# Optimization experiments

Hardware: AMD Instinct MI355X
Metric: run time of the kernel (lower is better)

The kernel has to match this reference:

```python
import jax, jax.numpy as jnp
import numpy as np


def setup_inputs() -> dict:
    key = jax.random.key(0)
    ks = jax.random.split(key, 10)
    B, L, H, T = 512, 30, 1024, 30
    k = 1.0 / np.sqrt(H).astype(np.float32)
    input_hidden = jax.random.normal(ks[0], (B, L, H), jnp.float32)
    tgt = jax.random.normal(ks[1], (B, T, H), jnp.float32)
    # all entries valid (no -1 padding): guarantees every row always has an
    # unmasked slot so softmax never sees an all -inf row (the torch code NaNs there)
    pos_label = jax.random.randint(ks[2], (B, L), 0, L)
    S = jax.random.uniform(ks[3], (H,), jnp.float32)            # torch.rand init
    W_ih = jax.random.uniform(ks[4], (3 * H, H), jnp.float32, -k, k)
    W_hh = jax.random.uniform(ks[5], (3 * H, H), jnp.float32, -k, k)
    b_ih = jax.random.uniform(ks[6], (3 * H,), jnp.float32, -k, k)
    b_hh = jax.random.uniform(ks[7], (3 * H,), jnp.float32, -k, k)
    Wl_w = jax.random.uniform(ks[8], (H, H), jnp.float32, -k, k)
    Wl_b = jax.random.uniform(ks[9], (H,), jnp.float32, -k, k)
    return dict(input_hidden=input_hidden, tgt=tgt, pos_label=pos_label,
                max_length=30, S=S, W_ih=W_ih, W_hh=W_hh, b_ih=b_ih, b_hh=b_hh,
                Wl_w=Wl_w, Wl_b=Wl_b)


def reference(input_hidden, tgt, pos_label, max_length, S, W_ih, W_hh, b_ih, b_hh, Wl_w, Wl_b):
    # teacher_forcing_ratio = 1.0, generate = False (training path of Plan_GRU)
    B, L, H = input_hidden.shape
    T = max_length
    ss = (pos_label != -1).sum(axis=1)                     # [B] valid prefix length
    valid = jnp.arange(L)[None, :] < ss[:, None]           # [B, L]

    def gru_cell(x, h):
        gi = x @ W_ih.T + b_ih                             # [B, 3H]
        gh = h @ W_hh.T + b_hh
        ir, iz, inn = jnp.split(gi, 3, axis=-1)
        hr, hz, hn = jnp.split(gh, 3, axis=-1)
        r = jax.nn.sigmoid(ir + hr)
        z = jax.nn.sigmoid(iz + hz)
        n = jnp.tanh(inn + r * hn)
        return (1.0 - z) * n + z * h

    h0 = input_hidden.mean(axis=1)                         # [B, H]
    x0 = jnp.broadcast_to(S, (B, H))
    # input at step 0 is S; at step i>0 it is tgt[:, i-1] (teacher forcing)
    xs = jnp.concatenate([x0[:, None, :], tgt[:, :T - 1]], axis=1).transpose(1, 0, 2)  # [T,B,H]
    flag0 = jnp.zeros((B, L), jnp.bool_)

    def step(carry, x):
        h, flag = carry
        h = gru_cell(x, h)                                 # [B, H]
        pre = jnp.einsum('bh,blh->bl', h @ Wl_w.T + Wl_b, input_hidden)  # [B, L]
        masked = jnp.where(flag | ~valid, -jnp.inf, jax.lax.stop_gradient(pre))
        top = jax.nn.softmax(masked, axis=1)
        am = jnp.argmax(top, axis=1)                       # [B]
        flag = flag | (jnp.arange(L)[None, :] == am[:, None])
        return (h, flag), (pre, top)

    (_, _), (preds, infer) = jax.lax.scan(step, (h0, flag0), xs)
    outputs = preds.transpose(1, 0, 2)                     # [B, T, L]
    pre_inf = jax.lax.stop_gradient(infer.transpose(1, 0, 2))
    return outputs, pre_inf
```

## Files before the change

### kernel.cpp

```cpp
#include <hip/hip_runtime.h>

#define Bsz 512
#define Lsz 30
#define Hsz 1024
#define Tsz 30

typedef _Float16 f16;
typedef f16 f16x8 __attribute__((ext_vector_type(8)));
typedef unsigned short u16x8 __attribute__((ext_vector_type(8)));
typedef float  f32x4  __attribute__((ext_vector_type(4)));
typedef unsigned int u32;
typedef unsigned short u16;

#define WSCALE 32.0f
#define INVWS  0.03125f
#define INV2   0.0009765625f

__device__ __forceinline__ u16 h2u(f16 h) {
  union { f16 h; u16 u; } v; v.h = h; return v.u;
}
__device__ __forceinline__ f16x8 ld8h(const u16* p) {
  return *reinterpret_cast<const f16x8*>(p);
}
__device__ __forceinline__ void stage16(const u16* g, u16* l) {
  __builtin_amdgcn_global_load_lds(
      (const __attribute__((address_space(1))) u32*)g,
      (__attribute__((address_space(3))) u32*)l, 16, 0, 0);
}

__global__ __launch_bounds__(256) void k_split(
    const float* __restrict__ src, u16* __restrict__ hi,
    u16* __restrict__ lo, int n4)
{
  const int i = blockIdx.x * 256 + threadIdx.x;
  if (i >= n4) return;
  const float4 v = ((const float4*)src)[i];
  const float f[4] = { v.x * WSCALE, v.y * WSCALE, v.z * WSCALE, v.w * WSCALE };
  u16 h[4], l[4];
  #pragma unroll
  for (int j = 0; j < 4; ++j) {
    const f16 hb = (f16)f[j];
    const f16 lb = (f16)(f[j] - (float)hb);
    h[j] = h2u(hb); l[j] = h2u(lb);
  }
  ((ushort4*)hi)[i] = make_ushort4(h[0], h[1], h[2], h[3]);
  ((ushort4*)lo)[i] = make_ushort4(l[0], l[1], l[2], l[3]);
}

__global__ __launch_bounds__(256) void k_splitT2(
    const float* __restrict__ src, u16* __restrict__ t0, u16* __restrict__ t1)
{
  __shared__ float t[32][33];
  const int tid = threadIdx.x;
  const int bi = blockIdx.x * 32, bj = blockIdx.y * 32;
  const int r = tid >> 3, c4 = (tid & 7) * 4;
  const float4 v = *(const float4*)(src + (size_t)(bi + r) * Hsz + bj + c4);
  t[r][c4] = v.x; t[r][c4 + 1] = v.y; t[r][c4 + 2] = v.z; t[r][c4 + 3] = v.w;
  __syncthreads();
  u16 h[4], l[4];
  #pragma unroll
  for (int i = 0; i < 4; ++i) {
    const float f = t[c4 + i][r] * WSCALE;
    const f16 hb = (f16)f;
    const f16 lb = (f16)(f - (float)hb);
    h[i] = h2u(hb); l[i] = h2u(lb);
  }
  const size_t o = (size_t)(bj + r) * Hsz + bi + c4;
  *(ushort4*)(t0 + o) = make_ushort4(h[0], h[1], h[2], h[3]);
  *(ushort4*)(t1 + o) = make_ushort4(l[0], l[1], l[2], l[3]);
}

__global__ __launch_bounds__(256) void k_init(
    const float* __restrict__ ih, const int* __restrict__ pos,
    const float* __restrict__ wlb,
    float* __restrict__ hf, u16* __restrict__ hh,
    u16* __restrict__ hl, float* __restrict__ c0,
    u32* __restrict__ valid)
{
  __shared__ float red[4];
  const int b = blockIdx.x, tid = threadIdx.x;
  const int lane = tid & 63, wid = tid >> 6;
  const float4 wb = ((const float4*)wlb)[tid];
  float s0 = 0.f, s1 = 0.f, s2 = 0.f, s3 = 0.f;
  for (int l = 0; l < Lsz; ++l) {
    const float4 v = ((const float4*)(ih + ((size_t)b * Lsz + l) * Hsz))[tid];
    s0 += v.x; s1 += v.y; s2 += v.z; s3 += v.w;
    float part = v.x * wb.x + v.y * wb.y + v.z * wb.z + v.w * wb.w;
    #pragma unroll
    for (int off = 32; off >= 1; off >>= 1) part += __shfl_xor(part, off, 64);
    if (lane == 0) red[wid] = part;
    __syncthreads();
    if (tid == 0) c0[b * Lsz + l] = red[0] + red[1] + red[2] + red[3];
    __syncthreads();
  }
  const size_t o = (size_t)b * Hsz + tid * 4;
  const float m[4] = { s0 / 30.f, s1 / 30.f, s2 / 30.f, s3 / 30.f };
  *(float4*)(hf + o) = make_float4(m[0], m[1], m[2], m[3]);
  u16 h4[4], l4[4];
  #pragma unroll
  for (int j = 0; j < 4; ++j) {
    const float hs = m[j] * WSCALE;
    const f16 hb = (f16)hs;
    const f16 lb = (f16)(hs - (float)hb);
    h4[j] = h2u(hb); l4[j] = h2u(lb);
  }
  *(ushort4*)(hh + o) = make_ushort4(h4[0], h4[1], h4[2], h4[3]);
  *(ushort4*)(hl + o) = make_ushort4(l4[0], l4[1], l4[2], l4[3]);
  if (tid == 0) {
    int ss = 0;
    for (int l = 0; l < Lsz; ++l) ss += (pos[b * Lsz + l] != -1) ? 1 : 0;
    valid[b] = (ss >= 32) ? 0xFFFFFFFFu : ((1u << ss) - 1u);
  }
}

__global__ __launch_bounds__(256) void k_gemv0(
    const float* __restrict__ S, const float* __restrict__ wih,
    float* __restrict__ gi0)
{
  const int n = blockIdx.x * 64 + (threadIdx.x >> 2);
  const int part = threadIdx.x & 3;
  const float4* s4 = (const float4*)S + part * 64;
  const float4* w4 = (const float4*)(wih + (size_t)n * Hsz) + part * 64;
  float s = 0.f;
  #pragma unroll 8
  for (int i = 0; i < 64; ++i) {
    const float4 a = s4[i], b = w4[i];
    s = fmaf(a.x, b.x, s); s = fmaf(a.y, b.y, s);
    s = fmaf(a.z, b.z, s); s = fmaf(a.w, b.w, s);
  }
  s += __shfl_xor(s, 1, 64);
  s += __shfl_xor(s, 2, 64);
  if (part == 0) gi0[n] = s;
}

template<int MODE>
__global__ __launch_bounds__(256) void k_tgemm(
    const float* __restrict__ Afp,
    const u16* __restrict__ Bh, const u16* __restrict__ Bl,
    float* __restrict__ C, u16* __restrict__ Ch, u16* __restrict__ Cl,
    int ldc, int t0)
{
  constexpr int oAh = 0, oAl = 4096, oBh = 8192, oBl = 12288;
  __shared__ u16 lds[2][16384];

  const int tid = threadIdx.x;
  const int w = tid >> 6, lane = tid & 63;
  const int wm = w >> 1, wn = w & 1;
  const int lr = lane & 15, lg = lane >> 4;

  const int nwg = gridDim.x * gridDim.y;
  int lin = blockIdx.y * gridDim.x + blockIdx.x;
  lin = (lin & 7) * (nwg >> 3) + (lin >> 3);
  const int bm = (lin / gridDim.x) * 128, bn = (lin % gridDim.x) * 128;

  const int ar = tid & 127, kh = tid >> 7;
  long arow;
  if (MODE == 1) arow = (long)((bm + ar) & 511) * Tsz + (t0 - 1) + ((bm + ar) >> 9);
  else           arow = bm + ar;
  const float* aptr = Afp + arow * Hsz + kh * 16;
  const int awo0 = (ar >> 4) * 512 + ((ar & 15) + 32 * kh) * 8;

  const u16* gpB[4]; int bwo[4];
  #pragma unroll
  for (int i = 0; i < 4; ++i) {
    const int cid = (w << 2) | i;
    const u16* base; int g, off;
    if (cid < 8) { base = Bh; g = cid;     off = oBh + g * 512; }
    else         { base = Bl; g = cid - 8; off = oBl + g * 512; }
    gpB[i] = base + (size_t)(bn + g * 16 + lr) * Hsz + lg * 8;
    bwo[i] = off;
  }

  float4 areg[4];
  #define LOAD_A() { _Pragma("unroll") for (int i = 0; i < 4; ++i) areg[i] = ((const float4*)aptr)[i]; aptr += 32; }
  #define STAGE_B(buf) { _Pragma("unroll") for (int i = 0; i < 4; ++i) { stage16(gpB[i], &lds[buf][bwo[i]]); gpB[i] += 32; } }
  #define WRITE_A(buf) { \
    u16x8 h0v, h1v, l0v, l1v; \
    _Pragma("unroll") for (int i = 0; i < 4; ++i) { \
      const float f[4] = { areg[i].x, areg[i].y, areg[i].z, areg[i].w }; \
      _Pragma("unroll") for (int c = 0; c < 4; ++c) { \
        const int j = 4 * i + c; \
        const f16 hb = (f16)f[c]; \
        const f16 lb = (f16)(f[c] - (float)hb); \
        if (j < 8) { h0v[j] = h2u(hb); l0v[j] = h2u(lb); } \
        else       { h1v[j - 8] = h2u(hb); l1v[j - 8] = h2u(lb); } \
      } \
    } \
    *(u16x8*)&lds[buf][oAh + awo0]       = h0v; \
    *(u16x8*)&lds[buf][oAh + awo0 + 128] = h1v; \
    *(u16x8*)&lds[buf][oAl + awo0]       = l0v; \
    *(u16x8*)&lds[buf][oAl + awo0 + 128] = l1v; }

  f32x4 acc[4][4] = {};

  LOAD_A();
  STAGE_B(0);
  WRITE_A(0);
  __syncthreads();

  for (int ks = 0; ks < 32; ++ks) {
    const int cur = ks & 1;
    if (ks < 31) { STAGE_B(cur ^ 1); LOAD_A(); }
    {
      const u16* L = &lds[cur][0];
      f16x8 a_h[4], a_l[4], b_h[4], b_l[4];
      #pragma unroll
      for (int m = 0; m < 4; ++m) {
        const int g = wm * 4 + m;
        a_h[m] = ld8h(L + oAh + g * 512 + lane * 8);
        a_l[m] = ld8h(L + oAl + g * 512 + lane * 8);
      }
      #pragma unroll
      for (int n = 0; n < 4; ++n) {
        const int g = wn * 4 + n;
        b_h[n] = ld8h(L + oBh + g * 512 + lane * 8);
        b_l[n] = ld8h(L + oBl + g * 512 + lane * 8);
      }
      #pragma unroll
      for (int m = 0; m < 4; ++m)
        #pragma unroll
        for (int n = 0; n < 4; ++n) {
          acc[m][n] = __builtin_amdgcn_mfma_f32_16x16x32_f16(a_h[m], b_h[n], acc[m][n], 0, 0, 0);
          acc[m][n] = __builtin_amdgcn_mfma_f32_16x16x32_f16(a_h[m], b_l[n], acc[m][n], 0, 0, 0);
          acc[m][n] = __builtin_amdgcn_mfma_f32_16x16x32_f16(a_l[m], b_h[n], acc[m][n], 0, 0, 0);
        }
    }
    __syncthreads();
    if (ks < 31) { WRITE_A(cur ^ 1); __syncthreads(); }
  }

  #pragma unroll
  for (int n = 0; n < 4; ++n) {
    const int col = bn + wn * 64 + n * 16 + lr;
    #pragma unroll
    for (int m = 0; m < 4; ++m) {
      #pragma unroll
      for (int rr = 0; rr < 4; ++rr) {
        const int row = bm + wm * 64 + m * 16 + lg * 4 + rr;
        if (MODE == 1) {
          const int slot = (t0 + (row >> 9)) & 7;
          C[((size_t)slot * Bsz + (row & 511)) * 3072 + col] = acc[m][n][rr] * INVWS;
        } else {
          const float v = acc[m][n][rr];
          const f16 hb = (f16)v;
          const f16 lb = (f16)(v - (float)hb);
          Ch[(size_t)row * ldc + col] = h2u(hb);
          Cl[(size_t)row * ldc + col] = h2u(lb);
        }
      }
    }
  }
  #undef LOAD_A
  #undef STAGE_B
  #undef WRITE_A
}

__global__ __launch_bounds__(512) void k_ghc(
    const u16* __restrict__ Hh, const u16* __restrict__ Hl,
    const u16* __restrict__ Wh, const u16* __restrict__ Wl,
    const float* __restrict__ gi, int gi_rs,
    const float* __restrict__ bih, const float* __restrict__ bhh,
    const float* __restrict__ hf_in, float* __restrict__ hf_out,
    u16* __restrict__ hho, u16* __restrict__ hlo,
    u16* __restrict__ Hph, u16* __restrict__ Hpl, int tstep)
{
  constexpr int oAh = 0, oAl = 2048, oBh = 4096, oBl = 7168;
  __shared__ u16 lds[2][10240];

  const int bn = (blockIdx.x & 31) * 32, bm = (blockIdx.x >> 5) * 64;
  const int tid = threadIdx.x;
  const int w = tid >> 6, lane = tid & 63;
  const int wm = w >> 1, wn = w & 1;
  const int lr = lane & 15, lg = lane >> 4;

  const u16* gp[3]; int ldso[3];
  const int nch = (w < 4) ? 3 : 2;
  #pragma unroll
  for (int i = 0; i < 3; ++i) {
    const int cid = w + 8 * i;
    if (cid >= 20) break;
    const u16* base; long row; int off;
    if (cid < 4)       { const int g = cid;      row = bm + g * 16 + lr;                         base = Hh; off = oAh + g * 512; }
    else if (cid < 8)  { const int g = cid - 4;  row = bm + g * 16 + lr;                         base = Hl; off = oAl + g * 512; }
    else if (cid < 14) { const int g = cid - 8;  row = (g >> 1) * 1024 + bn + (g & 1) * 16 + lr; base = Wh; off = oBh + g * 512; }
    else               { const int g = cid - 14; row = (g >> 1) * 1024 + bn + (g & 1) * 16 + lr; base = Wl; off = oBl + g * 512; }
    gp[i] = base + row * Hsz + lg * 8;
    ldso[i] = off;
  }

  f32x4 acc[3] = {};

  for (int i = 0; i < nch; ++i) { stage16(gp[i], &lds[0][ldso[i]]); gp[i] += 32; }
  __syncthreads();

  for (int ks = 0; ks < 32; ++ks) {
    const int cur = ks & 1;
    if (ks < 31) {
      for (int i = 0; i < nch; ++i) { stage16(gp[i], &lds[cur ^ 1][ldso[i]]); gp[i] += 32; }
    }
    const u16* L = &lds[cur][0];
    const f16x8 ah = ld8h(L + oAh + wm * 512 + lane * 8);
    const f16x8 al = ld8h(L + oAl + wm * 512 + lane * 8);
    #pragma unroll
    for (int gt = 0; gt < 3; ++gt) {
      const int g = gt * 2 + wn;
      const f16x8 bh = ld8h(L + oBh + g * 512 + lane * 8);
      const f16x8 bl = ld8h(L + oBl + g * 512 + lane * 8);
      acc[gt] = __builtin_amdgcn_mfma_f32_16x16x32_f16(ah, bh, acc[gt], 0, 0, 0);
      acc[gt] = __builtin_amdgcn_mfma_f32_16x16x32_f16(ah, bl, acc[gt], 0, 0, 0);
      acc[gt] = __builtin_amdgcn_mfma_f32_16x16x32_f16(al, bh, acc[gt], 0, 0, 0);
    }
    __syncthreads();
  }

  const int c = bn + wn * 16 + lr;
  const float b_ir = bih[c], b_iz = bih[1024 + c], b_in = bih[2048 + c];
  const float b_hr = bhh[c], b_hz = bhh[1024 + c], b_hn = bhh[2048 + c];
  #pragma unroll
  for (int rr = 0; rr < 4; ++rr) {
    const int row = bm + wm * 16 + lg * 4 + rr;
    const size_t gr = (size_t)row * gi_rs;
    const float pr = gi[gr + c]        + b_ir + acc[0][rr] * INV2 + b_hr;
    const float pz = gi[gr + 1024 + c] + b_iz + acc[1][rr] * INV2 + b_hz;
    const float r = 1.f / (1.f + expf(-pr));
    const float z = 1.f / (1.f + expf(-pz));
    const float n = tanhf(gi[gr + 2048 + c] + b_in + r * (acc[2][rr] * INV2 + b_hn));
    const size_t o = (size_t)row * Hsz + c;
    const float h = (1.f - z) * n + z * hf_in[o];
    hf_out[o] = h;
    const float hs = h * WSCALE;
    const f16 hb = (f16)hs;
    const f16 lb = (f16)(hs - (float)hb);
    hho[o] = h2u(hb);
    hlo[o] = h2u(lb);
    const size_t o2 = ((size_t)row * Tsz + tstep) * Hsz + c;
    Hph[o2] = h2u(hb);
    Hpl[o2] = h2u(lb);
  }
}

__global__ __launch_bounds__(256) void k_pre(
    const u16* __restrict__ Hph, const u16* __restrict__ Hpl,
    const u16* __restrict__ Gh, const u16* __restrict__ Gl,
    float* __restrict__ P)
{
  const int b = blockIdx.x;
  const int w = threadIdx.x >> 6, lane = threadIdx.x & 63;
  const int wm = w >> 1, wn = w & 1;
  const int lr = lane & 15, lg = lane >> 4;

  const int t_ = wm * 16 + lr;
  const int l_ = wn * 16 + lr;
  const size_t abase = ((size_t)b * Tsz + t_) * Hsz + lg * 8;
  const size_t bbase = ((size_t)b * Tsz + l_) * Hsz + lg * 8;

  f32x4 acc = {};
  for (int k0 = 0; k0 < Hsz; k0 += 32) {
    const f16x8 ah = ld8h(Hph + abase + k0);
    const f16x8 al = ld8h(Hpl + abase + k0);
    const f16x8 bh = ld8h(Gh + bbase + k0);
    const f16x8 bl = ld8h(Gl + bbase + k0);
    acc = __builtin_amdgcn_mfma_f32_16x16x32_f16(ah, bh, acc, 0, 0, 0);
    acc = __builtin_amdgcn_mfma_f32_16x16x32_f16(ah, bl, acc, 0, 0, 0);
    acc = __builtin_amdgcn_mfma_f32_16x16x32_f16(al, bh, acc, 0, 0, 0);
  }

  #pragma unroll
  for (int rr = 0; rr < 4; ++rr) {
    const int tr = wm * 16 + lg * 4 + rr;
    P[(size_t)b * 1024 + tr * 32 + wn * 16 + lr] = acc[rr] * INV2;
  }
}

__global__ __launch_bounds__(64) void k_sm(
    const float* __restrict__ P, const float* __restrict__ c0,
    const u32* __restrict__ valid, float* __restrict__ out)
{
  const int b = blockIdx.x;
  const int l = threadIdx.x;
  const bool act = (l < Lsz);
  const float c0l = act ? c0[b * Lsz + l] : 0.f;
  const u32 vmask = valid[b];
  u32 fl = 0;

  for (int t = 0; t < Tsz; ++t) {
    const float pre = act ? (P[(size_t)b * 1024 + t * 32 + l] + c0l) : 0.f;
    if (act) out[(size_t)b * (Tsz * Lsz) + t * Lsz + l] = pre;
    const u32 ex = fl | ~vmask;
    const bool ok = act && !((ex >> l) & 1u);
    const float v = ok ? pre : -3.4e38f;
    float best = v;
    #pragma unroll
    for (int off = 32; off >= 1; off >>= 1) best = fmaxf(best, __shfl_xor(best, off, 64));
    const unsigned long long msk = __ballot(v == best);
    const int am = __ffsll((long long)msk) - 1;
    const float e = ok ? expf(pre - best) : 0.f;
    float sum = e;
    #pragma unroll
    for (int off = 32; off >= 1; off >>= 1) sum += __shfl_xor(sum, off, 64);
    if (act)
      out[(size_t)Bsz * Tsz * Lsz + (size_t)b * (Tsz * Lsz) + t * Lsz + l] = e / sum;
    fl |= (1u << am);
  }
}

extern "C" void kernel_launch(void* const* d_in, const int* in_sizes, int n_in,
                              void* d_out, int out_size, void* d_ws, size_t ws_size,
                              hipStream_t stream) {
  const float* ih  = (const float*)d_in[0];
  const float* tg  = (const float*)d_in[1];
  const int*   pos = (const int*)d_in[2];
  const float* S   = (const float*)d_in[4];
  const float* wih = (const float*)d_in[5];
  const float* whh = (const float*)d_in[6];
  const float* bih = (const float*)d_in[7];
  const float* bhh = (const float*)d_in[8];
  const float* wlw = (const float*)d_in[9];
  const float* wlb = (const float*)d_in[10];
  float* out = (float*)d_out;

  const size_t NW3 = (size_t)3 * Hsz * Hsz;
  const size_t NW1 = (size_t)Hsz * Hsz;
  const size_t NH  = (size_t)Bsz * Hsz;
  const size_t NPL = ((size_t)Bsz * Tsz + 2) * Hsz;

  char* p = (char*)d_ws;
  u16* wihh = (u16*)p; p += NW3 * 2;
  u16* wihl = (u16*)p; p += NW3 * 2;
  u16* whhh = (u16*)p; p += NW3 * 2;
  u16* whhl = (u16*)p; p += NW3 * 2;
  u16* wlt0 = (u16*)p; p += NW1 * 2;
  u16* wlt1 = (u16*)p; p += NW1 * 2;
  float* ring = (float*)p; p += (size_t)8 * Bsz * 3072 * 4;
  u16* Gh  = (u16*)p; p += NPL * 2;
  u16* Gl  = (u16*)p; p += NPL * 2;
  u16* Hph = (u16*)p; p += NPL * 2;
  u16* Hpl = (u16*)p; p += NPL * 2;
  float* P   = (float*)p; p += (size_t)Bsz * 1024 * 4;
  float* c0  = (float*)p; p += (size_t)Bsz * Lsz * 4;
  float* gi0 = (float*)p; p += 3072 * 4;
  float* hfb[2]; u16* hhb[2]; u16* hlb[2];
  hfb[0] = (float*)p; p += NH * 4;
  hfb[1] = (float*)p; p += NH * 4;
  hhb[0] = (u16*)p; p += NH * 2;
  hlb[0] = (u16*)p; p += NH * 2;
  hhb[1] = (u16*)p; p += NH * 2;
  hlb[1] = (u16*)p; p += NH * 2;
  u32* valid = (u32*)p; p += Bsz * 4;

  k_split<<<(int)(NW3 / 4 + 255) / 256, 256, 0, stream>>>(wih, wihh, wihl, (int)(NW3 / 4));
  k_split<<<(int)(NW3 / 4 + 255) / 256, 256, 0, stream>>>(whh, whhh, whhl, (int)(NW3 / 4));
  k_splitT2<<<dim3(32, 32), 256, 0, stream>>>(wlw, wlt0, wlt1);
  k_init<<<Bsz, 256, 0, stream>>>(ih, pos, wlb, hfb[0], hhb[0], hlb[0], c0, valid);
  k_gemv0<<<48, 256, 0, stream>>>(S, wih, gi0);
  k_tgemm<0><<<dim3(8, 120), 256, 0, stream>>>(ih, wlt0, wlt1, nullptr, Gh, Gl, Hsz, 0);

  k_ghc<<<256, 512, 0, stream>>>(hhb[0], hlb[0], whhh, whhl, gi0, 0, bih, bhh,
                                 hfb[0], hfb[1], hhb[1], hlb[1], Hph, Hpl, 0);

  for (int t = 1; t < Tsz; ++t) {
    if (t == 1 || t == 9 || t == 17 || t == 25) {
      const int ns = (t == 25) ? 5 : 8;
      k_tgemm<1><<<dim3(24, ns * 4), 256, 0, stream>>>(tg, wihh, wihl, ring,
                                                       nullptr, nullptr, 3072, t);
    }
    const int ci = t & 1, ni = (t + 1) & 1;
    k_ghc<<<256, 512, 0, stream>>>(hhb[ci], hlb[ci], whhh, whhl,
                                   ring + (size_t)(t & 7) * Bsz * 3072, 3072,
                                   bih, bhh, hfb[ci], hfb[ni], hhb[ni], hlb[ni],
                                   Hph, Hpl, t);
  }

  k_pre<<<Bsz, 256, 0, stream>>>(Hph, Hpl, Gh, Gl, P);
  k_sm<<<Bsz, 64, 0, stream>>>(P, c0, valid, out);
}
```

Before: 1.701 ms.

## Fuse next-step input-gate GEMM into the recurrent GRU step kernel

Replaces the batched per-8-step input-projection GEMM launches with a combined step kernel. Blocks 0-255 run the recurrent hidden GEMM and GRU update for step t, and 96 extra blocks compute the input gates for step t+1 into the ring buffer. The aim is to fill idle CUs during the latency-bound recurrent step and remove separate large GEMM launches. In exchange the LDS allocation grows to the larger 16384-element buffer for all blocks, which may reduce occupancy of the recurrent blocks.

```diff
diff --git a/kernel.cpp b/kernel.cpp
--- a/kernel.cpp
+++ b/kernel.cpp
@@ -133,12 +133,10 @@
   if (part == 0) gi0[n] = s;
 }
 
-template<int MODE>
-__global__ __launch_bounds__(256) void k_tgemm(
+__global__ __launch_bounds__(256) void k_gemmG(
     const float* __restrict__ Afp,
     const u16* __restrict__ Bh, const u16* __restrict__ Bl,
-    float* __restrict__ C, u16* __restrict__ Ch, u16* __restrict__ Cl,
-    int ldc, int t0)
+    u16* __restrict__ Ch, u16* __restrict__ Cl)
 {
   constexpr int oAh = 0, oAl = 4096, oBh = 8192, oBl = 12288;
   __shared__ u16 lds[2][16384];
@@ -154,10 +152,7 @@
   const int bm = (lin / gridDim.x) * 128, bn = (lin % gridDim.x) * 128;
 
   const int ar = tid & 127, kh = tid >> 7;
-  long arow;
-  if (MODE == 1) arow = (long)((bm + ar) & 511) * Tsz + (t0 - 1) + ((bm + ar) >> 9);
-  else           arow = bm + ar;
-  const float* aptr = Afp + arow * Hsz + kh * 16;
+  const float* aptr = Afp + (size_t)(bm + ar) * Hsz + kh * 16;
   const int awo0 = (ar >> 4) * 512 + ((ar & 15) + 32 * kh) * 8;
 
   const u16* gpB[4]; int bwo[4];
@@ -237,16 +232,11 @@
       #pragma unroll
       for (int rr = 0; rr < 4; ++rr) {
         const int row = bm + wm * 64 + m * 16 + lg * 4 + rr;
-        if (MODE == 1) {
-          const int slot = (t0 + (row >> 9)) & 7;
-          C[((size_t)slot * Bsz + (row & 511)) * 3072 + col] = acc[m][n][rr] * INVWS;
-        } else {
-          const float v = acc[m][n][rr];
-          const f16 hb = (f16)v;
-          const f16 lb = (f16)(v - (float)hb);
-          Ch[(size_t)row * ldc + col] = h2u(hb);
-          Cl[(size_t)row * ldc + col] = h2u(lb);
-        }
+        const float v = acc[m][n][rr];
+        const f16 hb = (f16)v;
+        const f16 lb = (f16)(v - (float)hb);
+        Ch[(size_t)row * Hsz + col] = h2u(hb);
+        Cl[(size_t)row * Hsz + col] = h2u(lb);
       }
     }
   }
@@ -255,7 +245,8 @@
   #undef WRITE_A
 }
 
-__global__ __launch_bounds__(512) void k_ghc(
+__device__ __forceinline__ void ghc_body(
+    u16 (*lds)[16384],
     const u16* __restrict__ Hh, const u16* __restrict__ Hl,
     const u16* __restrict__ Wh, const u16* __restrict__ Wl,
     const float* __restrict__ gi, int gi_rs,
@@ -265,8 +256,6 @@
     u16* __restrict__ Hph, u16* __restrict__ Hpl, int tstep)
 {
   constexpr int oAh = 0, oAl = 2048, oBh = 4096, oBl = 7168;
-  __shared__ u16 lds[2][10240];
-
   const int bn = (blockIdx.x & 31) * 32, bm = (blockIdx.x >> 5) * 64;
   const int tid = threadIdx.x;
   const int w = tid >> 6, lane = tid & 63;
@@ -336,6 +325,120 @@
     const size_t o2 = ((size_t)row * Tsz + tstep) * Hsz + c;
     Hph[o2] = h2u(hb);
     Hpl[o2] = h2u(lb);
+  }
+}
+
+__device__ __forceinline__ void gi_body(
+    u16 (*lds)[16384],
+    const float* __restrict__ tg,
+    const u16* __restrict__ Bh, const u16* __restrict__ Bl,
+    float* __restrict__ ring, int ts, int gb)
+{
+  constexpr int oAh = 0, oAl = 4096, oBh = 8192, oBl = 12288;
+  const int tid = threadIdx.x;
+  const int w = tid >> 6, lane = tid & 63;
+  const int wm = w & 1, wn = w >> 1;
+  const int lr = lane & 15, lg = lane >> 4;
+  const int bm = (gb / 24) * 128, bn = (gb % 24) * 128;
+
+  const int ar = tid & 127, kh = tid >> 7;
+  const float* aptr = tg + ((size_t)(bm + ar) * Tsz + (ts - 1)) * Hsz + kh * 8;
+  const int awo = (ar >> 4) * 512 + ((ar & 15) + 16 * kh) * 8;
+
+  const u16* gpB[2]; int bwo[2];
+  #pragma unroll
+  for (int i = 0; i < 2; ++i) {
+    const int cid = w * 2 + i;
+    const u16* base; int g, off;
+    if (cid < 8) { base = Bh; g = cid;     off = oBh + g * 512; }
+    else         { base = Bl; g = cid - 8; off = oBl + g * 512; }
+    gpB[i] = base + (size_t)(bn + g * 16 + lr) * Hsz + lg * 8;
+    bwo[i] = off;
+  }
+
+  float4 a0, a1;
+  #define GI_LOAD_A() { a0 = ((const float4*)aptr)[0]; a1 = ((const float4*)aptr)[1]; aptr += 32; }
+  #define GI_STAGE_B(buf) { _Pragma("unroll") for (int i = 0; i < 2; ++i) { stage16(gpB[i], &lds[buf][bwo[i]]); gpB[i] += 32; } }
+  #define GI_WRITE_A(buf) { \
+    u16x8 hv, lv; \
+    const float f[8] = { a0.x, a0.y, a0.z, a0.w, a1.x, a1.y, a1.z, a1.w }; \
+    _Pragma("unroll") for (int j = 0; j < 8; ++j) { \
+      const f16 hb = (f16)f[j]; \
+      const f16 lb = (f16)(f[j] - (float)hb); \
+      hv[j] = h2u(hb); lv[j] = h2u(lb); \
+    } \
+    *(u16x8*)&lds[buf][oAh + awo] = hv; \
+    *(u16x8*)&lds[buf][oAl + awo] = lv; }
+
+  f32x4 acc[4][2] = {};
+
+  GI_LOAD_A();
+  GI_STAGE_B(0);
+  GI_WRITE_A(0);
+  __syncthreads();
+
+  for (int ks = 0; ks < 32; ++ks) {
+    const int cur = ks & 1;
+    if (ks < 31) { GI_STAGE_B(cur ^ 1); GI_LOAD_A(); }
+    {
+      const u16* L = &lds[cur][0];
+      f16x8 a_h[4], a_l[4], b_h[2], b_l[2];
+      #pragma unroll
+      for (int m = 0; m < 4; ++m) {
+        const int g = wm * 4 + m;
+        a_h[m] = ld8h(L + oAh + g * 512 + lane * 8);
+        a_l[m] = ld8h(L + oAl + g * 512 + lane * 8);
+      }
+      #pragma unroll
+      for (int n = 0; n < 2; ++n) {
+        const int g = wn * 2 + n;
+        b_h[n] = ld8h(L + oBh + g * 512 + lane * 8);
+        b_l[n] = ld8h(L + oBl + g * 512 + lane * 8);
+      }
+      #pragma unroll
+      for (int m = 0; m < 4; ++m)
+        #pragma unroll
+        for (int n = 0; n < 2; ++n) {
+          acc[m][n] = __builtin_amdgcn_mfma_f32_16x16x32_f16(a_h[m], b_h[n], acc[m][n], 0, 0, 0);
+          acc[m][n] = __builtin_amdgcn_mfma_f32_16x16x32_f16(a_h[m], b_l[n], acc[m][n], 0, 0, 0);
+          acc[m][n] = __builtin_amdgcn_mfma_f32_16x16x32_f16(a_l[m], b_h[n], acc[m][n], 0, 0, 0);
+        }
+    }
+    __syncthreads();
+    if (ks < 31) { GI_WRITE_A(cur ^ 1); __syncthreads(); }
+  }
+
+  const int slot = ts & 7;
+  #pragma unroll
+  for (int n = 0; n < 2; ++n) {
+    const int col = bn + wn * 32 + n * 16 + lr;
+    #pragma unroll
+    for (int m = 0; m < 4; ++m) {
+      #pragma unroll
+      for (int rr = 0; rr < 4; ++rr) {
+        const int row = bm + wm * 64 + m * 16 + lg * 4 + rr;
+        ring[((size_t)slot * Bsz + row) * 3072 + col] = acc[m][n][rr] * INVWS;
+      }
+    }
+  }
+  #undef GI_LOAD_A
+  #undef GI_STAGE_B
+  #undef GI_WRITE_A
+}
+
+__global__ __launch_bounds__(512) void k_step(
+    const u16* hh_t, const u16* hl_t, const u16* Wh, const u16* Wl,
+    const float* gi, int gi_rs, const float* bih, const float* bhh,
+    const float* hf_in, float* hf_out, u16* hh_n, u16* hl_n,
+    u16* Hph, u16* Hpl,
+    const float* tg, const u16* Wih_h, const u16* Wih_l, float* ring, int t)
+{
+  __shared__ u16 lds[2][16384];
+  if (blockIdx.x < 256) {
+    ghc_body(lds, hh_t, hl_t, Wh, Wl, gi, gi_rs, bih, bhh,
+             hf_in, hf_out, hh_n, hl_n, Hph, Hpl, t);
+  } else if (t + 1 < Tsz) {
+    gi_body(lds, tg, Wih_h, Wih_l, ring, t + 1, blockIdx.x - 256);
   }
 }
 
@@ -453,22 +556,16 @@
   k_splitT2<<<dim3(32, 32), 256, 0, stream>>>(wlw, wlt0, wlt1);
   k_init<<<Bsz, 256, 0, stream>>>(ih, pos, wlb, hfb[0], hhb[0], hlb[0], c0, valid);
   k_gemv0<<<48, 256, 0, stream>>>(S, wih, gi0);
-  k_tgemm<0><<<dim3(8, 120), 256, 0, stream>>>(ih, wlt0, wlt1, nullptr, Gh, Gl, Hsz, 0);
-
-  k_ghc<<<256, 512, 0, stream>>>(hhb[0], hlb[0], whhh, whhl, gi0, 0, bih, bhh,
-                                 hfb[0], hfb[1], hhb[1], hlb[1], Hph, Hpl, 0);
-
-  for (int t = 1; t < Tsz; ++t) {
-    if (t == 1 || t == 9 || t == 17 || t == 25) {
-      const int ns = (t == 25) ? 5 : 8;
-      k_tgemm<1><<<dim3(24, ns * 4), 256, 0, stream>>>(tg, wihh, wihl, ring,
-                                                       nullptr, nullptr, 3072, t);
-    }
+  k_gemmG<<<dim3(8, 120), 256, 0, stream>>>(ih, wlt0, wlt1, Gh, Gl);
+
+  for (int t = 0; t < Tsz; ++t) {
     const int ci = t & 1, ni = (t + 1) & 1;
-    k_ghc<<<256, 512, 0, stream>>>(hhb[ci], hlb[ci], whhh, whhl,
-                                   ring + (size_t)(t & 7) * Bsz * 3072, 3072,
-                                   bih, bhh, hfb[ci], hfb[ni], hhb[ni], hlb[ni],
-                                   Hph, Hpl, t);
+    const float* gip = (t == 0) ? gi0 : (ring + (size_t)(t & 7) * Bsz * 3072);
+    k_step<<<352, 512, 0, stream>>>(hhb[ci], hlb[ci], whhh, whhl,
+                                    gip, (t == 0) ? 0 : 3072, bih, bhh,
+                                    hfb[ci], hfb[ni], hhb[ni], hlb[ni],
+                                    Hph, Hpl,
+                                    tg, wihh, wihl, ring, t);
   }
 
   k_pre<<<Bsz, 256, 0, stream>>>(Hph, Hpl, Gh, Gl, P);
```

Measured after the change: 2.109 ms. 24.0% more time.

## Fuse input-gate GEMM into per-step GRU kernel and drop precomputed ring buffer

Applied to the files above, without the earlier changes.

Removes the batched input-projection GEMM (k_tgemm MODE 1) that wrote fp32 gate inputs into a ring buffer, and the step-0 GEMV. Each per-step GRU kernel now computes both x@W_ih and h@W_hh with split-fp16 MFMAs. A-operands are loaded straight from global memory into registers with prefetch, and only weights are staged in LDS. The tgt tensor is pre-split into fp16 hi/lo once, and S is broadcast into a hi/lo buffer. This removes ring-buffer traffic and extra launches, but doubles the MFMA work and the weight streaming inside the serial recurrent loop.

```diff
diff --git a/kernel.cpp b/kernel.cpp
--- a/kernel.cpp
+++ b/kernel.cpp
@@ -68,6 +68,24 @@
   const size_t o = (size_t)(bj + r) * Hsz + bi + c4;
   *(ushort4*)(t0 + o) = make_ushort4(h[0], h[1], h[2], h[3]);
   *(ushort4*)(t1 + o) = make_ushort4(l[0], l[1], l[2], l[3]);
+}
+
+__global__ __launch_bounds__(256) void k_x0(
+    const float* __restrict__ S, u16* __restrict__ xh, u16* __restrict__ xl)
+{
+  const int b = blockIdx.x, tid = threadIdx.x;
+  const float4 v = ((const float4*)S)[tid];
+  const float f[4] = { v.x * WSCALE, v.y * WSCALE, v.z * WSCALE, v.w * WSCALE };
+  u16 h[4], l[4];
+  #pragma unroll
+  for (int j = 0; j < 4; ++j) {
+    const f16 hb = (f16)f[j];
+    const f16 lb = (f16)(f[j] - (float)hb);
+    h[j] = h2u(hb); l[j] = h2u(lb);
+  }
+  const size_t o = (size_t)b * Hsz + tid * 4;
+  *(ushort4*)(xh + o) = make_ushort4(h[0], h[1], h[2], h[3]);
+  *(ushort4*)(xl + o) = make_ushort4(l[0], l[1], l[2], l[3]);
 }
 
 __global__ __launch_bounds__(256) void k_init(
@@ -113,32 +131,10 @@
   }
 }
 
-__global__ __launch_bounds__(256) void k_gemv0(
-    const float* __restrict__ S, const float* __restrict__ wih,
-    float* __restrict__ gi0)
-{
-  const int n = blockIdx.x * 64 + (threadIdx.x >> 2);
-  const int part = threadIdx.x & 3;
-  const float4* s4 = (const float4*)S + part * 64;
-  const float4* w4 = (const float4*)(wih + (size_t)n * Hsz) + part * 64;
-  float s = 0.f;
-  #pragma unroll 8
-  for (int i = 0; i < 64; ++i) {
-    const float4 a = s4[i], b = w4[i];
-    s = fmaf(a.x, b.x, s); s = fmaf(a.y, b.y, s);
-    s = fmaf(a.z, b.z, s); s = fmaf(a.w, b.w, s);
-  }
-  s += __shfl_xor(s, 1, 64);
-  s += __shfl_xor(s, 2, 64);
-  if (part == 0) gi0[n] = s;
-}
-
-template<int MODE>
-__global__ __launch_bounds__(256) void k_tgemm(
+__global__ __launch_bounds__(256) void k_gemmG(
     const float* __restrict__ Afp,
     const u16* __restrict__ Bh, const u16* __restrict__ Bl,
-    float* __restrict__ C, u16* __restrict__ Ch, u16* __restrict__ Cl,
-    int ldc, int t0)
+    u16* __restrict__ Ch, u16* __restrict__ Cl)
 {
   constexpr int oAh = 0, oAl = 4096, oBh = 8192, oBl = 12288;
   __shared__ u16 lds[2][16384];
@@ -154,10 +150,7 @@
   const int bm = (lin / gridDim.x) * 128, bn = (lin % gridDim.x) * 128;
 
   const int ar = tid & 127, kh = tid >> 7;
-  long arow;
-  if (MODE == 1) arow = (long)((bm + ar) & 511) * Tsz + (t0 - 1) + ((bm + ar) >> 9);
-  else           arow = bm + ar;
-  const float* aptr = Afp + arow * Hsz + kh * 16;
+  const float* aptr = Afp + (size_t)(bm + ar) * Hsz + kh * 16;
   const int awo0 = (ar >> 4) * 512 + ((ar & 15) + 32 * kh) * 8;
 
   const u16* gpB[4]; int bwo[4];
@@ -237,16 +230,11 @@
       #pragma unroll
       for (int rr = 0; rr < 4; ++rr) {
         const int row = bm + wm * 64 + m * 16 + lg * 4 + rr;
-        if (MODE == 1) {
-          const int slot = (t0 + (row >> 9)) & 7;
-          C[((size_t)slot * Bsz + (row & 511)) * 3072 + col] = acc[m][n][rr] * INVWS;
-        } else {
-          const float v = acc[m][n][rr];
-          const f16 hb = (f16)v;
-          const f16 lb = (f16)(v - (float)hb);
-          Ch[(size_t)row * ldc + col] = h2u(hb);
-          Cl[(size_t)row * ldc + col] = h2u(lb);
-        }
+        const float v = acc[m][n][rr];
+        const f16 hb = (f16)v;
+        const f16 lb = (f16)(v - (float)hb);
+        Ch[(size_t)row * Hsz + col] = h2u(hb);
+        Cl[(size_t)row * Hsz + col] = h2u(lb);
       }
     }
   }
@@ -255,17 +243,18 @@
   #undef WRITE_A
 }
 
-__global__ __launch_bounds__(512) void k_ghc(
+__global__ __launch_bounds__(512) void k_ghc2(
     const u16* __restrict__ Hh, const u16* __restrict__ Hl,
-    const u16* __restrict__ Wh, const u16* __restrict__ Wl,
-    const float* __restrict__ gi, int gi_rs,
+    const u16* __restrict__ Xh, const u16* __restrict__ Xl, int rmul, int radd,
+    const u16* __restrict__ WHh, const u16* __restrict__ WHl,
+    const u16* __restrict__ WIh, const u16* __restrict__ WIl,
     const float* __restrict__ bih, const float* __restrict__ bhh,
     const float* __restrict__ hf_in, float* __restrict__ hf_out,
     u16* __restrict__ hho, u16* __restrict__ hlo,
     u16* __restrict__ Hph, u16* __restrict__ Hpl, int tstep)
 {
-  constexpr int oAh = 0, oAl = 2048, oBh = 4096, oBl = 7168;
-  __shared__ u16 lds[2][10240];
+  constexpr int oWHh = 0, oWHl = 3072, oWIh = 6144, oWIl = 9216;
+  __shared__ u16 lds[2][12288];
 
   const int bn = (blockIdx.x & 31) * 32, bm = (blockIdx.x >> 5) * 64;
   const int tid = threadIdx.x;
@@ -274,43 +263,62 @@
   const int lr = lane & 15, lg = lane >> 4;
 
   const u16* gp[3]; int ldso[3];
-  const int nch = (w < 4) ? 3 : 2;
   #pragma unroll
   for (int i = 0; i < 3; ++i) {
     const int cid = w + 8 * i;
-    if (cid >= 20) break;
-    const u16* base; long row; int off;
-    if (cid < 4)       { const int g = cid;      row = bm + g * 16 + lr;                         base = Hh; off = oAh + g * 512; }
-    else if (cid < 8)  { const int g = cid - 4;  row = bm + g * 16 + lr;                         base = Hl; off = oAl + g * 512; }
-    else if (cid < 14) { const int g = cid - 8;  row = (g >> 1) * 1024 + bn + (g & 1) * 16 + lr; base = Wh; off = oBh + g * 512; }
-    else               { const int g = cid - 14; row = (g >> 1) * 1024 + bn + (g & 1) * 16 + lr; base = Wl; off = oBl + g * 512; }
+    const u16* base; int g, off;
+    if (cid < 6)       { g = cid;      base = WHh; off = oWHh + g * 512; }
+    else if (cid < 12) { g = cid - 6;  base = WHl; off = oWHl + g * 512; }
+    else if (cid < 18) { g = cid - 12; base = WIh; off = oWIh + g * 512; }
+    else               { g = cid - 18; base = WIl; off = oWIl + g * 512; }
+    const long row = (g >> 1) * 1024 + bn + (g & 1) * 16 + lr;
     gp[i] = base + row * Hsz + lg * 8;
     ldso[i] = off;
   }
 
-  f32x4 acc[3] = {};
-
-  for (int i = 0; i < nch; ++i) { stage16(gp[i], &lds[0][ldso[i]]); gp[i] += 32; }
+  const int rowA = bm + wm * 16 + lr;
+  const u16* hhp = Hh + (size_t)rowA * Hsz + lg * 8;
+  const u16* hlp = Hl + (size_t)rowA * Hsz + lg * 8;
+  const long xrow = (long)rowA * rmul + radd;
+  const u16* xhp = Xh + xrow * Hsz + lg * 8;
+  const u16* xlp = Xl + xrow * Hsz + lg * 8;
+
+  f32x4 acc[4] = {};
+
+  f16x8 cHh = ld8h(hhp), cHl = ld8h(hlp), cXh = ld8h(xhp), cXl = ld8h(xlp);
+  #pragma unroll
+  for (int i = 0; i < 3; ++i) { stage16(gp[i], &lds[0][ldso[i]]); gp[i] += 32; }
   __syncthreads();
 
   for (int ks = 0; ks < 32; ++ks) {
     const int cur = ks & 1;
+    f16x8 nHh, nHl, nXh, nXl;
     if (ks < 31) {
-      for (int i = 0; i < nch; ++i) { stage16(gp[i], &lds[cur ^ 1][ldso[i]]); gp[i] += 32; }
+      #pragma unroll
+      for (int i = 0; i < 3; ++i) { stage16(gp[i], &lds[cur ^ 1][ldso[i]]); gp[i] += 32; }
+      const int ko = (ks + 1) * 32;
+      nHh = ld8h(hhp + ko); nHl = ld8h(hlp + ko);
+      nXh = ld8h(xhp + ko); nXl = ld8h(xlp + ko);
     }
     const u16* L = &lds[cur][0];
-    const f16x8 ah = ld8h(L + oAh + wm * 512 + lane * 8);
-    const f16x8 al = ld8h(L + oAl + wm * 512 + lane * 8);
     #pragma unroll
     for (int gt = 0; gt < 3; ++gt) {
       const int g = gt * 2 + wn;
-      const f16x8 bh = ld8h(L + oBh + g * 512 + lane * 8);
-      const f16x8 bl = ld8h(L + oBl + g * 512 + lane * 8);
-      acc[gt] = __builtin_amdgcn_mfma_f32_16x16x32_f16(ah, bh, acc[gt], 0, 0, 0);
-      acc[gt] = __builtin_amdgcn_mfma_f32_16x16x32_f16(ah, bl, acc[gt], 0, 0, 0);
-      acc[gt] = __builtin_amdgcn_mfma_f32_16x16x32_f16(al, bh, acc[gt], 0, 0, 0);
+      const f16x8 bhh_ = ld8h(L + oWHh + g * 512 + lane * 8);
+      const f16x8 bhl_ = ld8h(L + oWHl + g * 512 + lane * 8);
+      const f16x8 bih_ = ld8h(L + oWIh + g * 512 + lane * 8);
+      const f16x8 bil_ = ld8h(L + oWIl + g * 512 + lane * 8);
+      const int ai = (gt == 2) ? 3 : gt;
+      const int xi = (gt == 2) ? 2 : gt;
+      acc[ai] = __builtin_amdgcn_mfma_f32_16x16x32_f16(cHh, bhh_, acc[ai], 0, 0, 0);
+      acc[ai] = __builtin_amdgcn_mfma_f32_16x16x32_f16(cHh, bhl_, acc[ai], 0, 0, 0);
+      acc[ai] = __builtin_amdgcn_mfma_f32_16x16x32_f16(cHl, bhh_, acc[ai], 0, 0, 0);
+      acc[xi] = __builtin_amdgcn_mfma_f32_16x16x32_f16(cXh, bih_, acc[xi], 0, 0, 0);
+      acc[xi] = __builtin_amdgcn_mfma_f32_16x16x32_f16(cXh, bil_, acc[xi], 0, 0, 0);
+      acc[xi] = __builtin_amdgcn_mfma_f32_16x16x32_f16(cXl, bih_, acc[xi], 0, 0, 0);
     }
     __syncthreads();
+    if (ks < 31) { cHh = nHh; cHl = nHl; cXh = nXh; cXl = nXl; }
   }
 
   const int c = bn + wn * 16 + lr;
@@ -319,12 +327,11 @@
   #pragma unroll
   for (int rr = 0; rr < 4; ++rr) {
     const int row = bm + wm * 16 + lg * 4 + rr;
-    const size_t gr = (size_t)row * gi_rs;
-    const float pr = gi[gr + c]        + b_ir + acc[0][rr] * INV2 + b_hr;
-    const float pz = gi[gr + 1024 + c] + b_iz + acc[1][rr] * INV2 + b_hz;
+    const float pr = acc[0][rr] * INV2 + b_ir + b_hr;
+    const float pz = acc[1][rr] * INV2 + b_iz + b_hz;
     const float r = 1.f / (1.f + expf(-pr));
     const float z = 1.f / (1.f + expf(-pz));
-    const float n = tanhf(gi[gr + 2048 + c] + b_in + r * (acc[2][rr] * INV2 + b_hn));
+    const float n = tanhf(acc[2][rr] * INV2 + b_in + r * (acc[3][rr] * INV2 + b_hn));
     const size_t o = (size_t)row * Hsz + c;
     const float h = (1.f - z) * n + z * hf_in[o];
     hf_out[o] = h;
@@ -422,6 +429,7 @@
   const size_t NW3 = (size_t)3 * Hsz * Hsz;
   const size_t NW1 = (size_t)Hsz * Hsz;
   const size_t NH  = (size_t)Bsz * Hsz;
+  const size_t NX  = (size_t)Bsz * Tsz * Hsz;
   const size_t NPL = ((size_t)Bsz * Tsz + 2) * Hsz;
 
   char* p = (char*)d_ws;
@@ -431,14 +439,16 @@
   u16* whhl = (u16*)p; p += NW3 * 2;
   u16* wlt0 = (u16*)p; p += NW1 * 2;
   u16* wlt1 = (u16*)p; p += NW1 * 2;
-  float* ring = (float*)p; p += (size_t)8 * Bsz * 3072 * 4;
-  u16* Gh  = (u16*)p; p += NPL * 2;
-  u16* Gl  = (u16*)p; p += NPL * 2;
-  u16* Hph = (u16*)p; p += NPL * 2;
-  u16* Hpl = (u16*)p; p += NPL * 2;
+  u16* xth  = (u16*)p; p += NX * 2;
+  u16* xtl  = (u16*)p; p += NX * 2;
+  u16* x0h  = (u16*)p; p += NH * 2;
+  u16* x0l  = (u16*)p; p += NH * 2;
+  u16* Gh   = (u16*)p; p += NPL * 2;
+  u16* Gl   = (u16*)p; p += NPL * 2;
+  u16* Hph  = (u16*)p; p += NPL * 2;
+  u16* Hpl  = (u16*)p; p += NPL * 2;
   float* P   = (float*)p; p += (size_t)Bsz * 1024 * 4;
   float* c0  = (float*)p; p += (size_t)Bsz * Lsz * 4;
-  float* gi0 = (float*)p; p += 3072 * 4;
   float* hfb[2]; u16* hhb[2]; u16* hlb[2];
   hfb[0] = (float*)p; p += NH * 4;
   hfb[1] = (float*)p; p += NH * 4;
@@ -450,25 +460,22 @@
 
   k_split<<<(int)(NW3 / 4 + 255) / 256, 256, 0, stream>>>(wih, wihh, wihl, (int)(NW3 / 4));
   k_split<<<(int)(NW3 / 4 + 255) / 256, 256, 0, stream>>>(whh, whhh, whhl, (int)(NW3 / 4));
+  k_split<<<(int)(NX / 4 + 255) / 256, 256, 0, stream>>>(tg, xth, xtl, (int)(NX / 4));
   k_splitT2<<<dim3(32, 32), 256, 0, stream>>>(wlw, wlt0, wlt1);
+  k_x0<<<Bsz, 256, 0, stream>>>(S, x0h, x0l);
   k_init<<<Bsz, 256, 0, stream>>>(ih, pos, wlb, hfb[0], hhb[0], hlb[0], c0, valid);
-  k_gemv0<<<48, 256, 0, stream>>>(S, wih, gi0);
-  k_tgemm<0><<<dim3(8, 120), 256, 0, stream>>>(ih, wlt0, wlt1, nullptr, Gh, Gl, Hsz, 0);
-
-  k_ghc<<<256, 512, 0, stream>>>(hhb[0], hlb[0], whhh, whhl, gi0, 0, bih, bhh,
-                                 hfb[0], hfb[1], hhb[1], hlb[1], Hph, Hpl, 0);
-
-  for (int t = 1; t < Tsz; ++t) {
-    if (t == 1 || t == 9 || t == 17 || t == 25) {
-      const int ns = (t == 25) ? 5 : 8;
-      k_tgemm<1><<<dim3(24, ns * 4), 256, 0, stream>>>(tg, wihh, wihl, ring,
-                                                       nullptr, nullptr, 3072, t);
-    }
+  k_gemmG<<<dim3(8, 120), 256, 0, stream>>>(ih, wlt0, wlt1, Gh, Gl);
+
+  for (int t = 0; t < Tsz; ++t) {
     const int ci = t & 1, ni = (t + 1) & 1;
-    k_ghc<<<256, 512, 0, stream>>>(hhb[ci], hlb[ci], whhh, whhl,
-                                   ring + (size_t)(t & 7) * Bsz * 3072, 3072,
-                                   bih, bhh, hfb[ci], hfb[ni], hhb[ni], hlb[ni],
-                                   Hph, Hpl, t);
+    const u16* xh = (t == 0) ? x0h : xth;
+    const u16* xl = (t == 0) ? x0l : xtl;
+    const int rmul = (t == 0) ? 1 : Tsz;
+    const int radd = (t == 0) ? 0 : (t - 1);
+    k_ghc2<<<256, 512, 0, stream>>>(hhb[ci], hlb[ci], xh, xl, rmul, radd,
+                                    whhh, whhl, wihh, wihl, bih, bhh,
+                                    hfb[ci], hfb[ni], hhb[ni], hlb[ni],
+                                    Hph, Hpl, t);
   }
 
   k_pre<<<Bsz, 256, 0, stream>>>(Hph, Hpl, Gh, Gl, P);
```

Result: slower. 2.131 ms, median of 2 (+25.3%).
